# Optimization experiments

Measured on AMD Instinct MI355X. Metric: run time of the kernel, lower is better.

Reference implementation:

```python
import jax, jax.numpy as jnp
import numpy as np

DEPTH = 4
HEADS = 8
DIM = 512
HID = 1024  # int(512 * 2.0)
P = 16
IMG = 224
GRID = IMG // P          # 14
NPATCH = GRID * GRID     # 196
NTOK = NPATCH + 1        # 197 (cls token)
BATCH = 64
EPS = 1e-5               # torch LayerNorm default


def layernorm(x, w, b):
    mu = jnp.mean(x, axis=-1, keepdims=True)
    var = jnp.mean(jnp.square(x - mu), axis=-1, keepdims=True)
    return (x - mu) * jax.lax.rsqrt(var + EPS) * w + b


def setup_inputs() -> dict:
    key = jax.random.key(0)
    ks = jax.random.split(key, 12)
    s = 0.02
    inp = {
        "x": jax.random.normal(ks[0], (BATCH, 3, IMG, IMG), jnp.float32),
        # patch-embed conv as matmul: kernel flattened in torch order (c, kh, kw)
        "conv_w": jax.random.normal(ks[1], (3 * P * P, DIM), jnp.float32) * s,
        "conv_b": jnp.zeros((DIM,), jnp.float32),
        "cls_token": jax.random.normal(ks[2], (1, 1, DIM), jnp.float32) * s,
        "pos_embed": jax.random.normal(ks[3], (1, NTOK, DIM), jnp.float32) * s,
        # per-block params stacked along depth
        "ln1_w": jnp.ones((DEPTH, DIM), jnp.float32),
        "ln1_b": jnp.zeros((DEPTH, DIM), jnp.float32),
        "qkv_w": jax.random.normal(ks[4], (DEPTH, DIM, 3 * DIM), jnp.float32) * s,
        "qkv_b": jnp.zeros((DEPTH, 3 * DIM), jnp.float32),
        "proj_w": jax.random.normal(ks[5], (DEPTH, DIM, DIM), jnp.float32) * s,
        "proj_b": jnp.zeros((DEPTH, DIM), jnp.float32),
        "ln2_w": jnp.ones((DEPTH, DIM), jnp.float32),
        "ln2_b": jnp.zeros((DEPTH, DIM), jnp.float32),
        "fc1_w": jax.random.normal(ks[6], (DEPTH, DIM, HID), jnp.float32) * s,
        "fc1_b": jnp.zeros((DEPTH, HID), jnp.float32),
        "fc2_w": jax.random.normal(ks[7], (DEPTH, HID, DIM), jnp.float32) * s,
        "fc2_b": jnp.zeros((DEPTH, DIM), jnp.float32),
        "norm_w": jnp.ones((DIM,), jnp.float32),
        "norm_b": jnp.zeros((DIM,), jnp.float32),
    }
    return inp


def reference(x, conv_w, conv_b, cls_token, pos_embed,
              ln1_w, ln1_b, qkv_w, qkv_b, proj_w, proj_b,
              ln2_w, ln2_b, fc1_w, fc1_b, fc2_w, fc2_b,
              norm_w, norm_b):
    B = x.shape[0]
    hd = DIM // HEADS
    scale = hd ** -0.5
    # PatchEmbed: conv with kernel=stride=patch == patch extraction + matmul
    patches = x.reshape(B, 3, GRID, P, GRID, P)
    patches = patches.transpose(0, 2, 4, 1, 3, 5).reshape(B, NPATCH, 3 * P * P)
    tok = patches @ conv_w + conv_b                      # [B, 196, DIM]
    cls = jnp.broadcast_to(cls_token, (B, 1, DIM))
    h = jnp.concatenate([cls, tok], axis=1) + pos_embed  # [B, 197, DIM]
    for i in range(DEPTH):
        # Attention block (eval mode: dropouts are identity)
        y = layernorm(h, ln1_w[i], ln1_b[i])
        qkv = (y @ qkv_w[i] + qkv_b[i]).reshape(B, NTOK, 3, HEADS, hd)
        qkv = qkv.transpose(2, 0, 3, 1, 4)               # [3, B, H, N, hd]
        q, k, v = qkv[0], qkv[1], qkv[2]
        attn = jax.nn.softmax(jnp.einsum('bhnd,bhmd->bhnm', q, k) * scale, axis=-1)
        o = jnp.einsum('bhnm,bhmd->bhnd', attn, v)
        o = o.transpose(0, 2, 1, 3).reshape(B, NTOK, DIM)
        h = h + (o @ proj_w[i] + proj_b[i])
        # MLP block (exact GELU as in torch nn.GELU)
        y = layernorm(h, ln2_w[i], ln2_b[i])
        y = jax.nn.gelu(y @ fc1_w[i] + fc1_b[i], approximate=False)
        h = h + (y @ fc2_w[i] + fc2_b[i])
    return layernorm(h, norm_w, norm_b)
```

## Files before the change

kernel.cpp:

```cpp
#include <hip/hip_runtime.h>
#include <hip/hip_bf16.h>

#define HEADS 8
#define DIM 512
#define HID 1024
#define NTOK 197
#define NPATCH 196
#define BATCH 64
#define MTOK (BATCH*NTOK)
#define MPATCH (BATCH*NPATCH)
#define KPATCH 768

typedef __attribute__((ext_vector_type(8))) short vbf8;
typedef __attribute__((ext_vector_type(4))) float vf4;

__device__ inline float bf2f(short u) {
  union { unsigned int i; float f; } v; v.i = ((unsigned int)(unsigned short)u) << 16; return v.f;
}
__device__ inline short f2bf(float f) {
  union { float f; unsigned int i; } u; u.f = f;
  unsigned int r = u.i + 0x7fffu + ((u.i >> 16) & 1u);
  return (short)(r >> 16);
}

__device__ inline void gl_lds16(const void* g, void* l) {
  __builtin_amdgcn_global_load_lds(
      (const __attribute__((address_space(1))) void*)g,
      (__attribute__((address_space(3))) void*)l, 16, 0, 0);
}

__global__ void k_cvt_t(const float* __restrict__ in, short* __restrict__ out, int K, int N) {
  int slice = blockIdx.z;
  in  += (size_t)slice * K * N;
  out += (size_t)slice * K * N;
  __shared__ short tile[64][72];
  int t = threadIdx.x;
  int k0 = blockIdx.y * 64, n0 = blockIdx.x * 64;
  int r = t >> 2, c4 = (t & 3) << 4;
  #pragma unroll
  for (int j = 0; j < 16; j += 4) {
    float4 v = *(const float4*)(in + (size_t)(k0 + r) * N + n0 + c4 + j);
    tile[r][c4 + j + 0] = f2bf(v.x);
    tile[r][c4 + j + 1] = f2bf(v.y);
    tile[r][c4 + j + 2] = f2bf(v.z);
    tile[r][c4 + j + 3] = f2bf(v.w);
  }
  __syncthreads();
  int n = t >> 2, kc = (t & 3) << 4;
  vbf8 a, b;
  #pragma unroll
  for (int j = 0; j < 8; ++j) a[j] = tile[kc + j][n];
  #pragma unroll
  for (int j = 0; j < 8; ++j) b[j] = tile[kc + 8 + j][n];
  *(vbf8*)(out + (size_t)(n0 + n) * K + k0 + kc) = a;
  *(vbf8*)(out + (size_t)(n0 + n) * K + k0 + kc + 8) = b;
}

__global__ void k_im2col(const float* __restrict__ x, short* __restrict__ patches) {
  int tid = blockIdx.x * 256 + threadIdx.x;
  if (tid >= MPATCH * 48) return;
  int b = tid / (NPATCH * 48);
  int r = tid % (NPATCH * 48);
  int p = r / 48;
  int ck = r % 48;
  int c = ck >> 4, kh = ck & 15;
  int gy = p / 14, gx = p % 14;
  const float* src = x + ((size_t)((b * 3 + c) * 224) + gy * 16 + kh) * 224 + gx * 16;
  short* dst = patches + (size_t)(b * NPATCH + p) * KPATCH + c * 256 + kh * 16;
  float4 v0 = *(const float4*)(src);
  float4 v1 = *(const float4*)(src + 4);
  float4 v2 = *(const float4*)(src + 8);
  float4 v3 = *(const float4*)(src + 12);
  vbf8 o0, o1;
  o0[0]=f2bf(v0.x); o0[1]=f2bf(v0.y); o0[2]=f2bf(v0.z); o0[3]=f2bf(v0.w);
  o0[4]=f2bf(v1.x); o0[5]=f2bf(v1.y); o0[6]=f2bf(v1.z); o0[7]=f2bf(v1.w);
  o1[0]=f2bf(v2.x); o1[1]=f2bf(v2.y); o1[2]=f2bf(v2.z); o1[3]=f2bf(v2.w);
  o1[4]=f2bf(v3.x); o1[5]=f2bf(v3.y); o1[6]=f2bf(v3.z); o1[7]=f2bf(v3.w);
  *(vbf8*)dst = o0;
  *(vbf8*)(dst + 8) = o1;
}

__global__ void k_cls(const float* __restrict__ cls, const float* __restrict__ pos,
                      float* __restrict__ h) {
  int b = blockIdx.x, t = threadIdx.x;
  float* hr = h + (size_t)b * NTOK * DIM;
  hr[t]       = cls[t]       + pos[t];
  hr[t + 256] = cls[t + 256] + pos[t + 256];
}

template<int OUTBF>
__global__ __launch_bounds__(256) void k_ln(const float* __restrict__ x,
                                            const float* __restrict__ w,
                                            const float* __restrict__ b,
                                            void* __restrict__ out) {
  int wid = threadIdx.x >> 6, lane = threadIdx.x & 63;
  int row = blockIdx.x * 4 + wid;
  const float* xr = x + (size_t)row * DIM + lane * 8;
  float4 va = *(const float4*)xr;
  float4 vb = *(const float4*)(xr + 4);
  float s  = va.x + va.y + va.z + va.w + vb.x + vb.y + vb.z + vb.w;
  float ss = va.x*va.x + va.y*va.y + va.z*va.z + va.w*va.w
           + vb.x*vb.x + vb.y*vb.y + vb.z*vb.z + vb.w*vb.w;
  #pragma unroll
  for (int o = 32; o > 0; o >>= 1) { s += __shfl_xor(s, o); ss += __shfl_xor(ss, o); }
  float mu = s * (1.0f / DIM);
  float var = ss * (1.0f / DIM) - mu * mu;
  float rs = rsqrtf(var + 1e-5f);
  float4 wa = *(const float4*)(w + lane * 8);
  float4 wb = *(const float4*)(w + lane * 8 + 4);
  float4 ba = *(const float4*)(b + lane * 8);
  float4 bb = *(const float4*)(b + lane * 8 + 4);
  float y0 = (va.x - mu) * rs * wa.x + ba.x;
  float y1 = (va.y - mu) * rs * wa.y + ba.y;
  float y2 = (va.z - mu) * rs * wa.z + ba.z;
  float y3 = (va.w - mu) * rs * wa.w + ba.w;
  float y4 = (vb.x - mu) * rs * wb.x + bb.x;
  float y5 = (vb.y - mu) * rs * wb.y + bb.y;
  float y6 = (vb.z - mu) * rs * wb.z + bb.z;
  float y7 = (vb.w - mu) * rs * wb.w + bb.w;
  if (OUTBF) {
    vbf8 pk;
    pk[0]=f2bf(y0); pk[1]=f2bf(y1); pk[2]=f2bf(y2); pk[3]=f2bf(y3);
    pk[4]=f2bf(y4); pk[5]=f2bf(y5); pk[6]=f2bf(y6); pk[7]=f2bf(y7);
    *(vbf8*)((short*)out + (size_t)row * DIM + lane * 8) = pk;
  } else {
    float4 oa, ob;
    oa.x=y0; oa.y=y1; oa.z=y2; oa.w=y3;
    ob.x=y4; ob.y=y5; ob.z=y6; ob.w=y7;
    float* op = (float*)out + (size_t)row * DIM + lane * 8;
    *(float4*)op = oa;
    *(float4*)(op + 4) = ob;
  }
}

template<int MODE, int MF>
__global__ __launch_bounds__(256) void k_gemm(
    const short* __restrict__ A, const short* __restrict__ Bt,
    const float* __restrict__ bias, void* __restrict__ out,
    const float* __restrict__ extra, int M, int N, int K)
{
  constexpr int BM = MF * 32;
  __shared__ short As[2][BM * 64];
  __shared__ short Bs[2][128 * 64];
  int gx = gridDim.x;
  int nwg = gx * gridDim.y;
  int orig = blockIdx.y * gx + blockIdx.x;
  int q = nwg >> 3, r = nwg & 7, xcd = orig & 7, off = orig >> 3;
  int nid = (xcd < r ? xcd * (q + 1) : r * (q + 1) + (xcd - r) * q) + off;
  int bm = nid / gx, bn = nid % gx;

  int t = threadIdx.x, wid = t >> 6, lane = t & 63;
  int wm = wid >> 1, wn = wid & 1;
  int lr = lane & 15, lk = lane >> 4;
  int srow = lane >> 3;
  int scol = (lane & 7) * 8;

  const short* Abase = A  + (size_t)(bm * BM  + srow) * K + scol;
  const short* Bbase = Bt + (size_t)(bn * 128 + srow) * K + scol;

  auto stage = [&](int buf, int k0) {
    #pragma unroll
    for (int i = 0; i < MF; ++i) {
      int rc = wid * MF + i;
      gl_lds16(Abase + (size_t)(rc * 8) * K + k0, &As[buf][rc * 512]);
    }
    #pragma unroll
    for (int i = 0; i < 4; ++i) {
      int rc = wid * 4 + i;
      gl_lds16(Bbase + (size_t)(rc * 8) * K + k0, &Bs[buf][rc * 512]);
    }
  };

  vf4 acc[MF][4];
  #pragma unroll
  for (int i = 0; i < MF; ++i)
    #pragma unroll
    for (int j = 0; j < 4; ++j) {
      acc[i][j][0] = 0.f; acc[i][j][1] = 0.f; acc[i][j][2] = 0.f; acc[i][j][3] = 0.f;
    }

  int nt = K >> 6;
  stage(0, 0);
  __syncthreads();
  int cur = 0;
  for (int tt = 0; tt < nt; ++tt) {
    if (tt + 1 < nt) stage(cur ^ 1, (tt + 1) << 6);
    #pragma unroll
    for (int s = 0; s < 2; ++s) {
      vbf8 af[MF], bfr[4];
      #pragma unroll
      for (int i = 0; i < MF; ++i)
        af[i] = *(const vbf8*)&As[cur][(wm * (BM / 2) + i * 16 + lr) * 64 + s * 32 + lk * 8];
      #pragma unroll
      for (int j = 0; j < 4; ++j)
        bfr[j] = *(const vbf8*)&Bs[cur][(wn * 64 + j * 16 + lr) * 64 + s * 32 + lk * 8];
      #pragma unroll
      for (int i = 0; i < MF; ++i)
        #pragma unroll
        for (int j = 0; j < 4; ++j)
          acc[i][j] = __builtin_amdgcn_mfma_f32_16x16x32_bf16(af[i], bfr[j], acc[i][j], 0, 0, 0);
    }
    __syncthreads();
    cur ^= 1;
  }

  int rbase = bm * BM + wm * (BM / 2);
  int cbase = bn * 128 + wn * 64;
  #pragma unroll
  for (int i = 0; i < MF; ++i) {
    #pragma unroll
    for (int j = 0; j < 4; ++j) {
      int col = cbase + j * 16 + lr;
      float bs = bias[col];
      #pragma unroll
      for (int z = 0; z < 4; ++z) {
        int row = rbase + i * 16 + lk * 4 + z;
        if (row < M) {
          float v = acc[i][j][z] + bs;
          if (MODE == 0) {
            ((short*)out)[(size_t)row * N + col] = f2bf(v);
          } else if (MODE == 1) {
            float g = 0.5f * v * (1.f + erff(v * 0.70710678118f));
            ((short*)out)[(size_t)row * N + col] = f2bf(g);
          } else if (MODE == 2) {
            float* hp = (float*)out + (size_t)row * N + col;
            *hp = *hp + v;
          } else {
            int b_ = row / NPATCH, p = row - b_ * NPATCH;
            ((float*)out)[((size_t)b_ * NTOK + 1 + p) * DIM + col] =
                v + extra[(size_t)(1 + p) * DIM + col];
          }
        }
      }
    }
  }
}

#define VSTR 232
__global__ __launch_bounds__(256) void k_attn(const short* __restrict__ qkv,
                                              short* __restrict__ o) {
  int h = blockIdx.x, b = blockIdx.y;
  __shared__ short Vt[64 * VSTR];
  __shared__ short Pt[4][16 * VSTR];
  int t = threadIdx.x, wid = t >> 6, lane = t & 63;
  int lq = lane & 15, g4 = lane >> 4;
  const size_t base = (size_t)(b * NTOK) * 1536 + h * 64;

  vbf8 vz;
  #pragma unroll
  for (int j = 0; j < 8; ++j) vz[j] = 0;
  for (int idx = t; idx < 224 * 8; idx += 256) {
    int r = idx >> 3, c8 = idx & 7;
    vbf8 v = vz;
    if (r < NTOK) v = *(const vbf8*)(qkv + base + (size_t)r * 1536 + 1024 + c8 * 8);
    int cs = r ^ ((c8 & 3) << 3);
    #pragma unroll
    for (int j = 0; j < 8; ++j) Vt[(c8 * 8 + j) * VSTR + cs] = v[j];
  }
  __syncthreads();

  short* Pw = &Pt[wid][0];
  for (int qt = wid; qt < 13; qt += 4) {
    const short* qp = qkv + base + (size_t)(qt * 16 + lq) * 1536 + g4 * 8;
    vbf8 qf0 = *(const vbf8*)qp;
    vbf8 qf1 = *(const vbf8*)(qp + 32);
    float sc[13][4];
    #pragma unroll
    for (int kt = 0; kt < 13; ++kt) {
      const short* kp = qkv + base + (size_t)(kt * 16 + lq) * 1536 + 512 + g4 * 8;
      vbf8 kf0 = *(const vbf8*)kp;
      vbf8 kf1 = *(const vbf8*)(kp + 32);
      vf4 s; s[0] = 0.f; s[1] = 0.f; s[2] = 0.f; s[3] = 0.f;
      s = __builtin_amdgcn_mfma_f32_16x16x32_bf16(kf0, qf0, s, 0, 0, 0);
      s = __builtin_amdgcn_mfma_f32_16x16x32_bf16(kf1, qf1, s, 0, 0, 0);
      #pragma unroll
      for (int z = 0; z < 4; ++z) {
        int krow = kt * 16 + g4 * 4 + z;
        sc[kt][z] = (krow < NTOK) ? s[z] * 0.125f : -1e30f;
      }
    }
    float mx = -1e30f;
    #pragma unroll
    for (int kt = 0; kt < 13; ++kt)
      #pragma unroll
      for (int z = 0; z < 4; ++z) mx = fmaxf(mx, sc[kt][z]);
    mx = fmaxf(mx, __shfl_xor(mx, 16));
    mx = fmaxf(mx, __shfl_xor(mx, 32));
    float sum = 0.f;
    #pragma unroll
    for (int kt = 0; kt < 13; ++kt)
      #pragma unroll
      for (int z = 0; z < 4; ++z) {
        float e = __expf(sc[kt][z] - mx);
        sc[kt][z] = e;
        sum += e;
      }
    sum += __shfl_xor(sum, 16);
    sum += __shfl_xor(sum, 32);
    float inv = 1.f / sum;
    #pragma unroll
    for (int kt = 0; kt < 13; ++kt) {
      *(short4*)&Pw[lq * VSTR + kt * 16 + g4 * 4] =
          make_short4(f2bf(sc[kt][0]), f2bf(sc[kt][1]), f2bf(sc[kt][2]), f2bf(sc[kt][3]));
    }
    *(short4*)&Pw[lq * VSTR + 208 + g4 * 4] = make_short4(0, 0, 0, 0);
    vf4 oacc[4];
    #pragma unroll
    for (int dt = 0; dt < 4; ++dt) { oacc[dt][0]=0.f; oacc[dt][1]=0.f; oacc[dt][2]=0.f; oacc[dt][3]=0.f; }
    #pragma unroll
    for (int u = 0; u < 7; ++u) {
      vbf8 pb = *(const vbf8*)&Pw[lq * VSTR + u * 32 + g4 * 8];
      #pragma unroll
      for (int dt = 0; dt < 4; ++dt) {
        int swz = ((dt * 2 + (lq >> 3)) & 3) << 3;
        vbf8 va = *(const vbf8*)&Vt[(dt * 16 + lq) * VSTR + ((u * 32 + g4 * 8) ^ swz)];
        oacc[dt] = __builtin_amdgcn_mfma_f32_16x16x32_bf16(va, pb, oacc[dt], 0, 0, 0);
      }
    }
    int qrow = qt * 16 + lq;
    if (qrow < NTOK) {
      short* op = o + ((size_t)(b * NTOK) + qrow) * DIM + h * 64 + g4 * 4;
      #pragma unroll
      for (int dt = 0; dt < 4; ++dt)
        *(short4*)(op + dt * 16) = make_short4(f2bf(oacc[dt][0] * inv), f2bf(oacc[dt][1] * inv),
                                               f2bf(oacc[dt][2] * inv), f2bf(oacc[dt][3] * inv));
    }
  }
}

extern "C" void kernel_launch(void* const* d_in, const int* in_sizes, int n_in,
                              void* d_out, int out_size, void* d_ws, size_t ws_size,
                              hipStream_t stream) {
  (void)in_sizes; (void)n_in; (void)out_size; (void)ws_size;
  const float* x      = (const float*)d_in[0];
  const float* conv_w = (const float*)d_in[1];
  const float* conv_b = (const float*)d_in[2];
  const float* cls    = (const float*)d_in[3];
  const float* pos    = (const float*)d_in[4];
  const float* ln1_w  = (const float*)d_in[5];
  const float* ln1_b  = (const float*)d_in[6];
  const float* qkv_w  = (const float*)d_in[7];
  const float* qkv_b  = (const float*)d_in[8];
  const float* proj_w = (const float*)d_in[9];
  const float* proj_b = (const float*)d_in[10];
  const float* ln2_w  = (const float*)d_in[11];
  const float* ln2_b  = (const float*)d_in[12];
  const float* fc1_w  = (const float*)d_in[13];
  const float* fc1_b  = (const float*)d_in[14];
  const float* fc2_w  = (const float*)d_in[15];
  const float* fc2_b  = (const float*)d_in[16];
  const float* norm_w = (const float*)d_in[17];
  const float* norm_b = (const float*)d_in[18];

  short* conv_wT = (short*)d_ws;
  short* qkv_wT  = conv_wT + (size_t)512 * 768;
  short* proj_wT = qkv_wT  + (size_t)4 * 1536 * 512;
  short* fc1_wT  = proj_wT + (size_t)4 * 512 * 512;
  short* fc2_wT  = fc1_wT  + (size_t)4 * 512 * 1024;
  short* y_bf    = fc2_wT  + (size_t)4 * 1024 * 512;
  short* o_bf    = y_bf    + (size_t)MTOK * 512;
  short* big     = o_bf    + (size_t)MTOK * 512;
  float* h       = (float*)(big + (size_t)MTOK * 1536);

  k_cvt_t<<<dim3(8, 12, 1), 256, 0, stream>>>(conv_w, conv_wT, 768, 512);
  k_cvt_t<<<dim3(24, 8, 4), 256, 0, stream>>>(qkv_w, qkv_wT, 512, 1536);
  k_cvt_t<<<dim3(8, 8, 4), 256, 0, stream>>>(proj_w, proj_wT, 512, 512);
  k_cvt_t<<<dim3(16, 8, 4), 256, 0, stream>>>(fc1_w, fc1_wT, 512, 1024);
  k_cvt_t<<<dim3(8, 16, 4), 256, 0, stream>>>(fc2_w, fc2_wT, 1024, 512);

  k_im2col<<<2352, 256, 0, stream>>>(x, big);
  k_cls<<<64, 256, 0, stream>>>(cls, pos, h);
  k_gemm<3, 2><<<dim3(4, 196), 256, 0, stream>>>(big, conv_wT, conv_b, h, pos,
                                                 MPATCH, 512, 768);
  for (int i = 0; i < 4; ++i) {
    k_ln<1><<<MTOK / 4, 256, 0, stream>>>(h, ln1_w + i * 512, ln1_b + i * 512, y_bf);
    k_gemm<0, 4><<<dim3(12, 99), 256, 0, stream>>>(y_bf, qkv_wT + (size_t)i * 512 * 1536,
                                                   qkv_b + i * 1536, big, nullptr,
                                                   MTOK, 1536, 512);
    k_attn<<<dim3(8, 64), 256, 0, stream>>>(big, o_bf);
    k_gemm<2, 2><<<dim3(4, 197), 256, 0, stream>>>(o_bf, proj_wT + (size_t)i * 512 * 512,
                                                   proj_b + i * 512, h, nullptr,
                                                   MTOK, 512, 512);
    k_ln<1><<<MTOK / 4, 256, 0, stream>>>(h, ln2_w + i * 512, ln2_b + i * 512, y_bf);
    k_gemm<1, 4><<<dim3(8, 99), 256, 0, stream>>>(y_bf, fc1_wT + (size_t)i * 512 * 1024,
                                                  fc1_b + i * 1024, big, nullptr,
                                                  MTOK, 1024, 512);
    k_gemm<2, 2><<<dim3(4, 197), 256, 0, stream>>>(big, fc2_wT + (size_t)i * 1024 * 512,
                                                   fc2_b + i * 512, h, nullptr,
                                                   MTOK, 512, 1024);
  }
  k_ln<0><<<MTOK / 4, 256, 0, stream>>>(h, norm_w, norm_b, d_out);
}
```

Measured before the change: 1.011 ms.

## Single-buffer GEMM LDS with a swizzled staging layout to cut bank conflicts

The GEMM kernel drops its double-buffered shared-memory prefetch and uses one A/B tile buffer, loaded synchronously each k-step with a barrier before compute. Each lane's global load now maps to a different row-and-column arrangement inside the 8x64 chunk, and fragment reads use a matching offset. This is meant to remove LDS bank conflicts on the MFMA fragment reads and halve LDS use, which could raise occupancy. In exchange, global loads no longer overlap with the MFMA work.

```diff
diff --git a/kernel.cpp b/kernel.cpp
--- a/kernel.cpp
+++ b/kernel.cpp
@@ -140,8 +140,8 @@
     const float* __restrict__ extra, int M, int N, int K)
 {
   constexpr int BM = MF * 32;
-  __shared__ short As[2][BM * 64];
-  __shared__ short Bs[2][128 * 64];
+  __shared__ short As[BM * 64];
+  __shared__ short Bs[128 * 64];
   int gx = gridDim.x;
   int nwg = gx * gridDim.y;
   int orig = blockIdx.y * gx + blockIdx.x;
@@ -152,56 +152,49 @@
   int t = threadIdx.x, wid = t >> 6, lane = t & 63;
   int wm = wid >> 1, wn = wid & 1;
   int lr = lane & 15, lk = lane >> 4;
-  int srow = lane >> 3;
-  int scol = (lane & 7) * 8;
-
-  const short* Abase = A  + (size_t)(bm * BM  + srow) * K + scol;
-  const short* Bbase = Bt + (size_t)(bn * 128 + srow) * K + scol;
-
-  auto stage = [&](int buf, int k0) {
+
+  const size_t lane_off = (size_t)(lane & 7) * K + (lane >> 3) * 8;
+  const short* Abase = A  + (size_t)(bm * BM)  * K + lane_off;
+  const short* Bbase = Bt + (size_t)(bn * 128) * K + lane_off;
+
+  const int rdoff = (lr >> 3) * 512 + lk * 64 + (lr & 7) * 8;
+
+  vf4 acc[MF][4];
+  #pragma unroll
+  for (int i = 0; i < MF; ++i)
+    #pragma unroll
+    for (int j = 0; j < 4; ++j) {
+      acc[i][j][0] = 0.f; acc[i][j][1] = 0.f; acc[i][j][2] = 0.f; acc[i][j][3] = 0.f;
+    }
+
+  for (int k0 = 0; k0 < K; k0 += 64) {
+    if (k0) __syncthreads();
     #pragma unroll
     for (int i = 0; i < MF; ++i) {
       int rc = wid * MF + i;
-      gl_lds16(Abase + (size_t)(rc * 8) * K + k0, &As[buf][rc * 512]);
+      gl_lds16(Abase + (size_t)(rc * 8) * K + k0, &As[rc * 512]);
     }
     #pragma unroll
     for (int i = 0; i < 4; ++i) {
       int rc = wid * 4 + i;
-      gl_lds16(Bbase + (size_t)(rc * 8) * K + k0, &Bs[buf][rc * 512]);
-    }
-  };
-
-  vf4 acc[MF][4];
-  #pragma unroll
-  for (int i = 0; i < MF; ++i)
-    #pragma unroll
-    for (int j = 0; j < 4; ++j) {
-      acc[i][j][0] = 0.f; acc[i][j][1] = 0.f; acc[i][j][2] = 0.f; acc[i][j][3] = 0.f;
-    }
-
-  int nt = K >> 6;
-  stage(0, 0);
-  __syncthreads();
-  int cur = 0;
-  for (int tt = 0; tt < nt; ++tt) {
-    if (tt + 1 < nt) stage(cur ^ 1, (tt + 1) << 6);
+      gl_lds16(Bbase + (size_t)(rc * 8) * K + k0, &Bs[rc * 512]);
+    }
+    __syncthreads();
     #pragma unroll
     for (int s = 0; s < 2; ++s) {
       vbf8 af[MF], bfr[4];
       #pragma unroll
       for (int i = 0; i < MF; ++i)
-        af[i] = *(const vbf8*)&As[cur][(wm * (BM / 2) + i * 16 + lr) * 64 + s * 32 + lk * 8];
+        af[i] = *(const vbf8*)&As[(wm * (BM / 2) + i * 16) * 64 + s * 256 + rdoff];
       #pragma unroll
       for (int j = 0; j < 4; ++j)
-        bfr[j] = *(const vbf8*)&Bs[cur][(wn * 64 + j * 16 + lr) * 64 + s * 32 + lk * 8];
+        bfr[j] = *(const vbf8*)&Bs[(wn * 64 + j * 16) * 64 + s * 256 + rdoff];
       #pragma unroll
       for (int i = 0; i < MF; ++i)
         #pragma unroll
         for (int j = 0; j < 4; ++j)
           acc[i][j] = __builtin_amdgcn_mfma_f32_16x16x32_bf16(af[i], bfr[j], acc[i][j], 0, 0, 0);
     }
-    __syncthreads();
-    cur ^= 1;
   }
 
   int rbase = bm * BM + wm * (BM / 2);
```

New measurement: 1.058 ms. 1.05x slower.
